# Kernel tuning notes

Measured on AMD Instinct MI355X. Metric: run time of the kernel, lower is better.

## Reference

```python
import jax, jax.numpy as jnp
from jax import lax
import numpy as np

# geomloss SamplesLoss(loss='sinkhorn', p=2, blur=0.01, scaling=0.7, debias=True),
# tensorized backend, single scale. Sinkhorn divergence with eps-scaling annealing.
P = 2
BLUR = 0.01
SCALING = 0.7
# geomloss estimates the diameter from the data at runtime; for jit-compatibility we
# use a fixed upper bound appropriate for N(0,1) data in D=64 (max pair dist ~ 18).
DIAMETER = 20.0


def eps_schedule():
    # geomloss epsilon_schedule(p, diameter, blur, scaling)
    eps_list = [DIAMETER ** P]
    eps_list += [float(np.exp(e)) for e in np.arange(P * np.log(DIAMETER), P * np.log(BLUR), P * np.log(SCALING))]
    eps_list += [BLUR ** P]
    return eps_list


def sq_cost(x, y):
    # C(x,y) = |x-y|^2 / 2  (geomloss cost for p=2)
    x2 = jnp.sum(x * x, axis=-1)
    y2 = jnp.sum(y * y, axis=-1)
    return 0.5 * (x2[:, None] + y2[None, :] - 2.0 * (x @ y.T))


def softmin(eps, C, h):
    # -eps * log sum_j exp(h_j - C_ij/eps), stable logsumexp over rows
    return -eps * jax.nn.logsumexp(h[None, :] - C / eps, axis=1)


def sinkhorn_divergence(x, y):
    N, M = x.shape[0], y.shape[0]
    dt = x.dtype
    a_log = jnp.full((N,), -np.log(N), dtype=dt)  # uniform weights, log
    b_log = jnp.full((M,), -np.log(M), dtype=dt)

    C_xy = sq_cost(x, y)
    C_yx = C_xy.T
    C_xx = sq_cost(x, x)
    C_yy = sq_cost(y, y)
    # geomloss runs the annealing loop without autograd; detach the costs.
    Dxy, Dyx = lax.stop_gradient(C_xy), lax.stop_gradient(C_yx)
    Dxx, Dyy = lax.stop_gradient(C_xx), lax.stop_gradient(C_yy)

    eps_list = eps_schedule()
    eps = eps_list[0]
    f_ba = softmin(eps, Dxy, b_log)  # potential on x-points wrt beta
    g_ab = softmin(eps, Dyx, a_log)  # potential on y-points wrt alpha
    f_aa = softmin(eps, Dxx, a_log)  # debias: self potentials
    g_bb = softmin(eps, Dyy, b_log)

    for eps in eps_list:  # symmetric Sinkhorn updates with averaging
        ft = softmin(eps, Dxy, b_log + g_ab / eps)
        gt = softmin(eps, Dyx, a_log + f_ba / eps)
        f_ba, g_ab = 0.5 * (f_ba + ft), 0.5 * (g_ab + gt)
        f_aa = 0.5 * (f_aa + softmin(eps, Dxx, a_log + f_aa / eps))
        g_bb = 0.5 * (g_bb + softmin(eps, Dyy, b_log + g_bb / eps))

    # final extrapolation at eps = blur^p with detached potentials (grads flow via C)
    eps = eps_list[-1]
    sg = lax.stop_gradient
    f_ba_n = softmin(eps, C_xy, sg(b_log + g_ab / eps))
    g_ab_n = softmin(eps, C_yx, sg(a_log + f_ba / eps))
    f_aa_n = softmin(eps, C_xx, sg(a_log + f_aa / eps))
    g_bb_n = softmin(eps, C_yy, sg(b_log + g_bb / eps))

    a = jnp.exp(a_log)
    b = jnp.exp(b_log)
    # debiased: <a, f_ab - f_aa> + <b, g_ba - g_bb>
    return jnp.sum(a * (f_ba_n - f_aa_n)) + jnp.sum(b * (g_ab_n - g_bb_n))


def setup_inputs() -> dict:
    key = jax.random.key(0)
    k1, k2 = jax.random.split(key)
    latentSource = jax.random.normal(k1, (4096, 64), dtype=jnp.float32)
    latentTarget = jax.random.normal(k2, (4096, 64), dtype=jnp.float32)
    return {"latentSource": latentSource, "latentTarget": latentTarget}


def reference(latentSource, latentTarget):
    return sinkhorn_divergence(latentSource, latentTarget)
```

## Files before the change

### kernel.cpp

```cpp
#include <hip/hip_runtime.h>
#include <hip/hip_bf16.h>
#include <math.h>

#define NPTS 4096
#define KD   64
#define BR   64
#define BC   128
#define NSPLIT 4
#define CT   (NPTS / (BC * NSPLIT))
#define NTHREADS 256
#define BLOG  (-8.317766166719343f)
#define BLOG2 (-12.0f)
#define LOG2E 1.4426950408889634f
#define LN2   0.6931471805599453f

typedef __bf16 bf16x8 __attribute__((ext_vector_type(8)));
typedef float  f32x4  __attribute__((ext_vector_type(4)));

__device__ __forceinline__ float ex2(float x) {
#if __has_builtin(__builtin_amdgcn_exp2f)
  return __builtin_amdgcn_exp2f(x);
#else
  return exp2f(x);
#endif
}
__device__ __forceinline__ float lg2(float x) {
#if __has_builtin(__builtin_amdgcn_logf)
  return __builtin_amdgcn_logf(x);
#else
  return log2f(x);
#endif
}

struct FusedArgs {
  const unsigned short* X[4];
  const unsigned short* Y[4];
  const float* csq[4];
  const float* pmr[4];
  const float* psr[4];
  const float* potr[4];
  float* potw[4];
  float* pm;
  float* ps;
  float ie2;
  float elp;
  float alpha, beta;
  int mode;
};

__device__ __forceinline__ void gll16(const void* g, void* l) {
  __builtin_amdgcn_global_load_lds(
      (const __attribute__((address_space(1))) void*)g,
      (__attribute__((address_space(3))) void*)l, 16, 0, 0);
}

__global__ __launch_bounds__(NTHREADS, 4)
void fused_softmin(FusedArgs A) {
  __shared__ __align__(16) __bf16 YT[2][BC * KD];
  __shared__ __align__(16) float QL[BC * CT];

  const int tid  = threadIdx.x;
  const int lane = tid & 63;
  const int wave = tid >> 6;
  const int ln16 = lane & 15;
  const int rg   = lane >> 4;
  const int ln7  = ln16 & 7;
  const int rowblk = blockIdx.x;
  const int split  = blockIdx.y;
  const int dir    = blockIdx.z;

  const __bf16* __restrict__ Xb = (const __bf16*)A.X[dir];
  const __bf16* __restrict__ Yb = (const __bf16*)A.Y[dir];
  const float ie2 = A.ie2;
  const int row0 = rowblk * BR;
  const int col0 = split * (CT * BC);

  const int srow = tid >> 3;
  const int sseg = tid & 7;

#pragma unroll
  for (int it = 0; it < 4; ++it) {
    int r = it * 32 + srow;
    gll16(Yb + (size_t)(col0 + r) * KD + ((sseg ^ (r & 7)) << 3),
          (__bf16*)YT[0] + it * 2048 + wave * 512);
  }

  bf16x8 af[2];
  {
    const __bf16* ap = Xb + (size_t)(row0 + wave * 16 + ln16) * KD + rg * 8;
#pragma unroll
    for (int ks = 0; ks < 2; ++ks) {
      union { uint4 u; bf16x8 v; } t;
      t.u = *(const uint4*)(ap + ks * 32);
      af[ks] = t.v;
    }
  }

  {
    const float* __restrict__ csq = A.csq[dir];
    if (A.mode == 0) {
#pragma unroll
      for (int i = 0; i < 4; ++i) {
        int c = col0 + tid + i * 256;
        QL[tid + i * 256] = BLOG2 - csq[c] * ie2;
      }
    } else {
      const float* __restrict__ pmr = A.pmr[dir];
      const float* __restrict__ psr = A.psr[dir];
      const float* __restrict__ potr = A.potr[dir];
      float* __restrict__ potw = A.potw[dir];
#pragma unroll
      for (int i = 0; i < 4; ++i) {
        int c = col0 + tid + i * 256;
        float m0 = pmr[0 * NPTS + c], m1 = pmr[1 * NPTS + c];
        float m2 = pmr[2 * NPTS + c], m3 = pmr[3 * NPTS + c];
        float s0 = psr[0 * NPTS + c], s1 = psr[1 * NPTS + c];
        float s2 = psr[2 * NPTS + c], s3 = psr[3 * NPTS + c];
        float m4 = fmaxf(fmaxf(m0, m1), fmaxf(m2, m3));
        float s4 = s0 * ex2(m0 - m4) + s1 * ex2(m1 - m4) +
                   s2 * ex2(m2 - m4) + s3 * ex2(m3 - m4);
        float lse2 = m4 + lg2(s4);
        float xsq = csq[c];
        float v = xsq - A.elp * lse2;
        float g = A.alpha * potr[c] + A.beta * v;
        if (rowblk == 0) potw[c] = g;
        QL[tid + i * 256] = BLOG2 + (g - xsq) * ie2;
      }
    }
  }

  float m[4], s[4];
#pragma unroll
  for (int r = 0; r < 4; ++r) { m[r] = -__builtin_inff(); s[r] = 0.f; }

  const __bf16* xbase_unused = nullptr; (void)xbase_unused;
  __syncthreads();

  for (int tile = 0; tile < CT; ++tile) {
    const int cb = tile & 1;

    if (tile < CT - 1) {
      const int nc0 = col0 + (tile + 1) * BC;
#pragma unroll
      for (int it = 0; it < 4; ++it) {
        int r = it * 32 + srow;
        gll16(Yb + (size_t)(nc0 + r) * KD + ((sseg ^ (r & 7)) << 3),
              (__bf16*)YT[cb ^ 1] + it * 2048 + wave * 512);
      }
    }

    float qv[8];
#pragma unroll
    for (int t = 0; t < 8; ++t) qv[t] = QL[tile * BC + t * 16 + ln16];

    f32x4 acc[8];
#pragma unroll
    for (int t = 0; t < 8; ++t)
#pragma unroll
      for (int i = 0; i < 4; ++i) acc[t][i] = 0.f;

    const __bf16* ybase = YT[cb] + ln16 * KD;
#pragma unroll
    for (int ks = 0; ks < 2; ++ks) {
      const int p = ((ks << 2) | rg) ^ ln7;
#pragma unroll
      for (int t = 0; t < 8; ++t) {
        union { uint4 u; bf16x8 v; } bb;
        bb.u = *(const uint4*)(ybase + t * 16 * KD + p * 8);
        acc[t] = __builtin_amdgcn_mfma_f32_16x16x32_bf16(af[ks], bb.v, acc[t], 0, 0, 0);
      }
    }

#pragma unroll
    for (int r = 0; r < 4; ++r) {
      float l[8];
#pragma unroll
      for (int t = 0; t < 8; ++t) l[t] = fmaf(acc[t][r], ie2, qv[t]);
      float tmax = -__builtin_inff();
#pragma unroll
      for (int t = 0; t < 8; ++t) tmax = fmaxf(tmax, l[t]);
      float mn = fmaxf(m[r], tmax);
      float sadd = 0.f;
#pragma unroll
      for (int t = 0; t < 8; ++t) sadd += ex2(l[t] - mn);
      s[r] = fmaf(s[r], ex2(m[r] - mn), sadd);
      m[r] = mn;
    }
    __syncthreads();
  }

#pragma unroll
  for (int r = 0; r < 4; ++r) {
#pragma unroll
    for (int d = 1; d < 16; d <<= 1) {
      float mo = __shfl_xor(m[r], d, 64);
      float so = __shfl_xor(s[r], d, 64);
      float mn = fmaxf(m[r], mo);
      s[r] = ex2(m[r] - mn) * s[r] + ex2(mo - mn) * so;
      m[r] = mn;
    }
  }
  if (ln16 == 0) {
#pragma unroll
    for (int r = 0; r < 4; ++r) {
      int row = row0 + wave * 16 + rg * 4 + r;
      size_t gi = (size_t)(dir * NSPLIT + split) * NPTS + row;
      A.pm[gi] = m[r];
      A.ps[gi] = s[r];
    }
  }
}

__global__ void prep(const float* __restrict__ x, const float* __restrict__ y,
                     float* xs, float* ys,
                     unsigned short* xb, unsigned short* yb) {
  int gid = blockIdx.x * blockDim.x + threadIdx.x;
  int isx = (gid < NPTS) ? 1 : 0;
  const float* p = isx ? x : y;
  int row = gid & (NPTS - 1);
  const float4* r4 = (const float4*)(p + (size_t)row * KD);
  unsigned short* ob = (isx ? xb : yb) + (size_t)row * KD;
  float s = 0.f;
#pragma unroll
  for (int i = 0; i < 16; ++i) {
    float4 v = r4[i];
    s += v.x * v.x + v.y * v.y + v.z * v.z + v.w * v.w;
    union { __bf16 h[4]; uint2 u; } t;
    t.h[0] = (__bf16)v.x; t.h[1] = (__bf16)v.y;
    t.h[2] = (__bf16)v.z; t.h[3] = (__bf16)v.w;
    *(uint2*)(ob + i * 4) = t.u;
  }
  (isx ? xs : ys)[row] = 0.5f * s;
}

__global__ void final_reduce(const float* __restrict__ pm,
                             const float* __restrict__ ps,
                             const float* __restrict__ xsx,
                             const float* __restrict__ xsy,
                             float elpF, float* out) {
  __shared__ float red[256];
  int t = threadIdx.x;
  float acc = 0.f;
  for (int r = t; r < NPTS; r += 256) {
#pragma unroll
    for (int d = 0; d < 4; ++d) {
      float m0 = pm[(size_t)(d * NSPLIT + 0) * NPTS + r];
      float m1 = pm[(size_t)(d * NSPLIT + 1) * NPTS + r];
      float m2 = pm[(size_t)(d * NSPLIT + 2) * NPTS + r];
      float m3 = pm[(size_t)(d * NSPLIT + 3) * NPTS + r];
      float s0 = ps[(size_t)(d * NSPLIT + 0) * NPTS + r];
      float s1 = ps[(size_t)(d * NSPLIT + 1) * NPTS + r];
      float s2 = ps[(size_t)(d * NSPLIT + 2) * NPTS + r];
      float s3 = ps[(size_t)(d * NSPLIT + 3) * NPTS + r];
      float m4 = fmaxf(fmaxf(m0, m1), fmaxf(m2, m3));
      float s4 = s0 * ex2(m0 - m4) + s1 * ex2(m1 - m4) +
                 s2 * ex2(m2 - m4) + s3 * ex2(m3 - m4);
      float lse2 = m4 + lg2(s4);
      float xsq = (d == 0 || d == 2) ? xsx[r] : xsy[r];
      float f = xsq - elpF * lse2;
      acc += (d < 2) ? f : -f;
    }
  }
  red[t] = acc;
  __syncthreads();
  for (int off = 128; off > 0; off >>= 1) {
    if (t < off) red[t] += red[t + off];
    __syncthreads();
  }
  if (t == 0) out[0] = red[0] * (1.0f / NPTS);
}

extern "C" void kernel_launch(void* const* d_in, const int* in_sizes, int n_in,
                              void* d_out, int out_size, void* d_ws, size_t ws_size,
                              hipStream_t stream) {
  const float* x = (const float*)d_in[0];
  const float* y = (const float*)d_in[1];
  float* out = (float*)d_out;
  float* w = (float*)d_ws;

  float* xs_x = w;
  float* xs_y = w + NPTS;
  float* pot0 = w + 2 * NPTS;
  float* pot1 = w + 6 * NPTS;
  float* pm0  = w + 10 * NPTS;
  float* ps0  = w + 26 * NPTS;
  float* pm1  = w + 42 * NPTS;
  float* ps1  = w + 58 * NPTS;
  unsigned short* xb = (unsigned short*)(w + 74 * NPTS);
  unsigned short* yb = (unsigned short*)(w + 106 * NPTS);
  float* pmb[2] = {pm0, pm1};
  float* psb[2] = {ps0, ps1};
  float* potb[2] = {pot0, pot1};

  double eps_list[32];
  int neps = 0;
  {
    double start = 2.0 * log(20.0);
    double stop  = 2.0 * log(0.01);
    double step  = 2.0 * log(0.7);
    eps_list[neps++] = 400.0;
    int cnt = (int)ceil((stop - start) / step);
    for (int i = 0; i < cnt && neps < 30; ++i) eps_list[neps++] = exp(start + (double)i * step);
    eps_list[neps++] = 1e-4;
  }

  const unsigned short* Xd[4] = {xb, yb, xb, yb};
  const unsigned short* Yd[4] = {yb, xb, xb, yb};
  const float* YSQd[4] = {xs_y, xs_x, xs_x, xs_y};
  const int qpair[4] = {1, 0, 2, 3};

  prep<<<dim3(32), dim3(256), 0, stream>>>(x, y, xs_x, xs_y, xb, yb);

  dim3 fgrid(NPTS / BR, NSPLIT, 4);

  double ecur[26];
  ecur[0] = eps_list[0];
  for (int k = 1; k <= 24; ++k) ecur[k] = eps_list[k - 1];
  ecur[25] = eps_list[neps - 1];

  for (int k = 0; k <= 25; ++k) {
    FusedArgs fa;
    for (int d = 0; d < 4; ++d) {
      fa.X[d] = Xd[d]; fa.Y[d] = Yd[d]; fa.csq[d] = YSQd[d];
      int p = qpair[d];
      fa.pmr[d]  = pmb[(k + 1) & 1] + (size_t)p * NSPLIT * NPTS;
      fa.psr[d]  = psb[(k + 1) & 1] + (size_t)p * NSPLIT * NPTS;
      fa.potr[d] = potb[(k + 1) & 1] + (size_t)p * NPTS;
      fa.potw[d] = potb[k & 1] + (size_t)p * NPTS;
    }
    fa.pm = pmb[k & 1];
    fa.ps = psb[k & 1];
    fa.ie2 = (float)(LOG2E / ecur[k]);
    fa.elp = (k == 0) ? 0.f : (float)(ecur[k - 1] * LN2);
    fa.alpha = (k <= 1) ? 0.f : 0.5f;
    fa.beta  = (k <= 1) ? 1.f : 0.5f;
    fa.mode  = (k == 0) ? 0 : 1;
    fused_softmin<<<fgrid, dim3(NTHREADS), 0, stream>>>(fa);
  }

  final_reduce<<<dim3(1), dim3(256), 0, stream>>>(
      pmb[25 & 1], psb[25 & 1], xs_x, xs_y,
      (float)(eps_list[neps - 1] * LN2), out);
}
```

Before: 636.8 us.

## Switch to 32x32x16 MFMA tiles and double row block per workgroup

The fused softmin kernel now uses 32x32x16 bf16 MFMA instructions instead of 16x16x32, and each wave covers 32 rows instead of 16, so the row block grows from 64 to 128. Each B fragment loaded from LDS now feeds more rows, which raises arithmetic intensity and halves the number of workgroups that reload the Y tiles. The online logsumexp state per lane grows to 16 rows and the cross-lane reduction widens to 32 lanes. This raises register pressure, so occupancy is lowered to 2 workgroups per CU, and the grid shrinks, which may underfill the GPU.

Result: slower. 750.4 us (+17.8%).

```diff
diff --git a/kernel.cpp b/kernel.cpp
--- a/kernel.cpp
+++ b/kernel.cpp
@@ -4,18 +4,17 @@
 
 #define NPTS 4096
 #define KD   64
-#define BR   64
+#define BR   128
 #define BC   128
 #define NSPLIT 4
 #define CT   (NPTS / (BC * NSPLIT))
 #define NTHREADS 256
-#define BLOG  (-8.317766166719343f)
 #define BLOG2 (-12.0f)
 #define LOG2E 1.4426950408889634f
 #define LN2   0.6931471805599453f
 
 typedef __bf16 bf16x8 __attribute__((ext_vector_type(8)));
-typedef float  f32x4  __attribute__((ext_vector_type(4)));
+typedef float  f32x16 __attribute__((ext_vector_type(16)));
 
 __device__ __forceinline__ float ex2(float x) {
 #if __has_builtin(__builtin_amdgcn_exp2f)
@@ -54,7 +53,7 @@
       (__attribute__((address_space(3))) void*)l, 16, 0, 0);
 }
 
-__global__ __launch_bounds__(NTHREADS, 4)
+__global__ __launch_bounds__(NTHREADS, 2)
 void fused_softmin(FusedArgs A) {
   __shared__ __align__(16) __bf16 YT[2][BC * KD];
   __shared__ __align__(16) float QL[BC * CT];
@@ -62,9 +61,9 @@
   const int tid  = threadIdx.x;
   const int lane = tid & 63;
   const int wave = tid >> 6;
-  const int ln16 = lane & 15;
-  const int rg   = lane >> 4;
-  const int ln7  = ln16 & 7;
+  const int ln   = lane & 31;
+  const int hh   = lane >> 5;
+  const int ln7  = ln & 7;
   const int rowblk = blockIdx.x;
   const int split  = blockIdx.y;
   const int dir    = blockIdx.z;
@@ -85,13 +84,13 @@
           (__bf16*)YT[0] + it * 2048 + wave * 512);
   }
 
-  bf16x8 af[2];
+  bf16x8 af[4];
   {
-    const __bf16* ap = Xb + (size_t)(row0 + wave * 16 + ln16) * KD + rg * 8;
-#pragma unroll
-    for (int ks = 0; ks < 2; ++ks) {
+    const __bf16* ap = Xb + (size_t)(row0 + wave * 32 + ln) * KD + hh * 8;
+#pragma unroll
+    for (int ks = 0; ks < 4; ++ks) {
       union { uint4 u; bf16x8 v; } t;
-      t.u = *(const uint4*)(ap + ks * 32);
+      t.u = *(const uint4*)(ap + ks * 16);
       af[ks] = t.v;
     }
   }
@@ -129,11 +128,10 @@
     }
   }
 
-  float m[4], s[4];
-#pragma unroll
-  for (int r = 0; r < 4; ++r) { m[r] = -__builtin_inff(); s[r] = 0.f; }
-
-  const __bf16* xbase_unused = nullptr; (void)xbase_unused;
+  float m[16], s[16];
+#pragma unroll
+  for (int r = 0; r < 16; ++r) { m[r] = -__builtin_inff(); s[r] = 0.f; }
+
   __syncthreads();
 
   for (int tile = 0; tile < CT; ++tile) {
@@ -149,40 +147,37 @@
       }
     }
 
-    float qv[8];
-#pragma unroll
-    for (int t = 0; t < 8; ++t) qv[t] = QL[tile * BC + t * 16 + ln16];
-
-    f32x4 acc[8];
-#pragma unroll
-    for (int t = 0; t < 8; ++t)
-#pragma unroll
-      for (int i = 0; i < 4; ++i) acc[t][i] = 0.f;
-
-    const __bf16* ybase = YT[cb] + ln16 * KD;
-#pragma unroll
-    for (int ks = 0; ks < 2; ++ks) {
-      const int p = ((ks << 2) | rg) ^ ln7;
-#pragma unroll
-      for (int t = 0; t < 8; ++t) {
+    float qv[4];
+#pragma unroll
+    for (int ct = 0; ct < 4; ++ct)
+      qv[ct] = QL[tile * BC + ct * 32 + ln];
+
+    f32x16 acc[4];
+#pragma unroll
+    for (int ct = 0; ct < 4; ++ct)
+#pragma unroll
+      for (int i = 0; i < 16; ++i) acc[ct][i] = 0.f;
+
+    const __bf16* ybase = YT[cb] + ln * KD;
+#pragma unroll
+    for (int ks = 0; ks < 4; ++ks) {
+      const int sg = ((ks << 1) | hh) ^ ln7;
+#pragma unroll
+      for (int ct = 0; ct < 4; ++ct) {
         union { uint4 u; bf16x8 v; } bb;
-        bb.u = *(const uint4*)(ybase + t * 16 * KD + p * 8);
-        acc[t] = __builtin_amdgcn_mfma_f32_16x16x32_bf16(af[ks], bb.v, acc[t], 0, 0, 0);
+        bb.u = *(const uint4*)(ybase + ct * 32 * KD + sg * 8);
+        acc[ct] = __builtin_amdgcn_mfma_f32_32x32x16_bf16(af[ks], bb.v, acc[ct], 0, 0, 0);
       }
     }
 
 #pragma unroll
-    for (int r = 0; r < 4; ++r) {
-      float l[8];
-#pragma unroll
-      for (int t = 0; t < 8; ++t) l[t] = fmaf(acc[t][r], ie2, qv[t]);
-      float tmax = -__builtin_inff();
-#pragma unroll
-      for (int t = 0; t < 8; ++t) tmax = fmaxf(tmax, l[t]);
-      float mn = fmaxf(m[r], tmax);
-      float sadd = 0.f;
-#pragma unroll
-      for (int t = 0; t < 8; ++t) sadd += ex2(l[t] - mn);
+    for (int r = 0; r < 16; ++r) {
+      float l0 = fmaf(acc[0][r], ie2, qv[0]);
+      float l1 = fmaf(acc[1][r], ie2, qv[1]);
+      float l2 = fmaf(acc[2][r], ie2, qv[2]);
+      float l3 = fmaf(acc[3][r], ie2, qv[3]);
+      float mn = fmaxf(m[r], fmaxf(fmaxf(l0, l1), fmaxf(l2, l3)));
+      float sadd = ex2(l0 - mn) + ex2(l1 - mn) + ex2(l2 - mn) + ex2(l3 - mn);
       s[r] = fmaf(s[r], ex2(m[r] - mn), sadd);
       m[r] = mn;
     }
@@ -190,9 +185,9 @@
   }
 
 #pragma unroll
-  for (int r = 0; r < 4; ++r) {
-#pragma unroll
-    for (int d = 1; d < 16; d <<= 1) {
+  for (int r = 0; r < 16; ++r) {
+#pragma unroll
+    for (int d = 1; d < 32; d <<= 1) {
       float mo = __shfl_xor(m[r], d, 64);
       float so = __shfl_xor(s[r], d, 64);
       float mn = fmaxf(m[r], mo);
@@ -200,10 +195,10 @@
       m[r] = mn;
     }
   }
-  if (ln16 == 0) {
-#pragma unroll
-    for (int r = 0; r < 4; ++r) {
-      int row = row0 + wave * 16 + rg * 4 + r;
+  if (ln == 0) {
+#pragma unroll
+    for (int r = 0; r < 16; ++r) {
+      int row = row0 + wave * 32 + (r & 3) + ((r >> 2) << 3) + (hh << 2);
       size_t gi = (size_t)(dir * NSPLIT + split) * NPTS + row;
       A.pm[gi] = m[r];
       A.ps[gi] = s[r];
```

## Reshape wave tiling to 32x64 per wave sharing B fragments across two row tiles

Applied to the files above, without the earlier changes.

Each wave now covers two 16-row tiles and half of the 128-column tile instead of one 16-row tile across all 128 columns. Each B fragment read from LDS feeds two MFMAs, which halves LDS reads per MFMA. Because the column halves are split across waves, the partial logsumexp count per row doubles from 4 to 8, so workspace, the merge step and the final reduce are widened to match. The launch bound is also switched to amdgpu_waves_per_eu(4,4). The cost is more per-lane register state and a larger partial merge.

Result: slower. 839.5 us (+31.8%).

```diff
diff --git a/kernel.cpp b/kernel.cpp
--- a/kernel.cpp
+++ b/kernel.cpp
@@ -7,9 +7,9 @@
 #define BR   64
 #define BC   128
 #define NSPLIT 4
+#define NPART  8
 #define CT   (NPTS / (BC * NSPLIT))
 #define NTHREADS 256
-#define BLOG  (-8.317766166719343f)
 #define BLOG2 (-12.0f)
 #define LOG2E 1.4426950408889634f
 #define LN2   0.6931471805599453f
@@ -54,7 +54,8 @@
       (__attribute__((address_space(3))) void*)l, 16, 0, 0);
 }
 
-__global__ __launch_bounds__(NTHREADS, 4)
+__global__ __launch_bounds__(NTHREADS)
+__attribute__((amdgpu_waves_per_eu(4, 4)))
 void fused_softmin(FusedArgs A) {
   __shared__ __align__(16) __bf16 YT[2][BC * KD];
   __shared__ __align__(16) float QL[BC * CT];
@@ -62,6 +63,8 @@
   const int tid  = threadIdx.x;
   const int lane = tid & 63;
   const int wave = tid >> 6;
+  const int rowgrp = wave >> 1;
+  const int half   = wave & 1;
   const int ln16 = lane & 15;
   const int rg   = lane >> 4;
   const int ln7  = ln16 & 7;
@@ -85,14 +88,15 @@
           (__bf16*)YT[0] + it * 2048 + wave * 512);
   }
 
-  bf16x8 af[2];
-  {
-    const __bf16* ap = Xb + (size_t)(row0 + wave * 16 + ln16) * KD + rg * 8;
+  bf16x8 af[2][2];
+#pragma unroll
+  for (int rt = 0; rt < 2; ++rt) {
+    const __bf16* ap = Xb + (size_t)(row0 + rowgrp * 32 + rt * 16 + ln16) * KD + rg * 8;
 #pragma unroll
     for (int ks = 0; ks < 2; ++ks) {
       union { uint4 u; bf16x8 v; } t;
       t.u = *(const uint4*)(ap + ks * 32);
-      af[ks] = t.v;
+      af[rt][ks] = t.v;
     }
   }
 
@@ -112,13 +116,17 @@
 #pragma unroll
       for (int i = 0; i < 4; ++i) {
         int c = col0 + tid + i * 256;
-        float m0 = pmr[0 * NPTS + c], m1 = pmr[1 * NPTS + c];
-        float m2 = pmr[2 * NPTS + c], m3 = pmr[3 * NPTS + c];
-        float s0 = psr[0 * NPTS + c], s1 = psr[1 * NPTS + c];
-        float s2 = psr[2 * NPTS + c], s3 = psr[3 * NPTS + c];
-        float m4 = fmaxf(fmaxf(m0, m1), fmaxf(m2, m3));
-        float s4 = s0 * ex2(m0 - m4) + s1 * ex2(m1 - m4) +
-                   s2 * ex2(m2 - m4) + s3 * ex2(m3 - m4);
+        float mv[NPART], sv[NPART];
+        float m4 = -__builtin_inff();
+#pragma unroll
+        for (int sp = 0; sp < NPART; ++sp) {
+          mv[sp] = pmr[sp * NPTS + c];
+          sv[sp] = psr[sp * NPTS + c];
+          m4 = fmaxf(m4, mv[sp]);
+        }
+        float s4 = 0.f;
+#pragma unroll
+        for (int sp = 0; sp < NPART; ++sp) s4 += sv[sp] * ex2(mv[sp] - m4);
         float lse2 = m4 + lg2(s4);
         float xsq = csq[c];
         float v = xsq - A.elp * lse2;
@@ -129,11 +137,12 @@
     }
   }
 
-  float m[4], s[4];
-#pragma unroll
-  for (int r = 0; r < 4; ++r) { m[r] = -__builtin_inff(); s[r] = 0.f; }
-
-  const __bf16* xbase_unused = nullptr; (void)xbase_unused;
+  float m[2][4], s[2][4];
+#pragma unroll
+  for (int rt = 0; rt < 2; ++rt)
+#pragma unroll
+    for (int r = 0; r < 4; ++r) { m[rt][r] = -__builtin_inff(); s[rt][r] = 0.f; }
+
   __syncthreads();
 
   for (int tile = 0; tile < CT; ++tile) {
@@ -149,65 +158,65 @@
       }
     }
 
-    float qv[8];
-#pragma unroll
-    for (int t = 0; t < 8; ++t) qv[t] = QL[tile * BC + t * 16 + ln16];
-
-    f32x4 acc[8];
-#pragma unroll
-    for (int t = 0; t < 8; ++t)
-#pragma unroll
-      for (int i = 0; i < 4; ++i) acc[t][i] = 0.f;
-
-    const __bf16* ybase = YT[cb] + ln16 * KD;
+    float qv[4];
+#pragma unroll
+    for (int ct = 0; ct < 4; ++ct)
+      qv[ct] = QL[tile * BC + half * 64 + ct * 16 + ln16];
+
+    f32x4 acc[2][4] = {};
+
+    const __bf16* yb0 = YT[cb] + (half * 64 + ln16) * KD;
 #pragma unroll
     for (int ks = 0; ks < 2; ++ks) {
       const int p = ((ks << 2) | rg) ^ ln7;
 #pragma unroll
-      for (int t = 0; t < 8; ++t) {
+      for (int ct = 0; ct < 4; ++ct) {
         union { uint4 u; bf16x8 v; } bb;
-        bb.u = *(const uint4*)(ybase + t * 16 * KD + p * 8);
-        acc[t] = __builtin_amdgcn_mfma_f32_16x16x32_bf16(af[ks], bb.v, acc[t], 0, 0, 0);
-      }
-    }
-
+        bb.u = *(const uint4*)(yb0 + ct * 16 * KD + p * 8);
+        acc[0][ct] = __builtin_amdgcn_mfma_f32_16x16x32_bf16(af[0][ks], bb.v, acc[0][ct], 0, 0, 0);
+        acc[1][ct] = __builtin_amdgcn_mfma_f32_16x16x32_bf16(af[1][ks], bb.v, acc[1][ct], 0, 0, 0);
+      }
+    }
+
+#pragma unroll
+    for (int rt = 0; rt < 2; ++rt)
+#pragma unroll
+      for (int r = 0; r < 4; ++r) {
+        float l0 = fmaf(acc[rt][0][r], ie2, qv[0]);
+        float l1 = fmaf(acc[rt][1][r], ie2, qv[1]);
+        float l2 = fmaf(acc[rt][2][r], ie2, qv[2]);
+        float l3 = fmaf(acc[rt][3][r], ie2, qv[3]);
+        float mn = fmaxf(m[rt][r], fmaxf(fmaxf(l0, l1), fmaxf(l2, l3)));
+        float sadd = ex2(l0 - mn) + ex2(l1 - mn) + ex2(l2 - mn) + ex2(l3 - mn);
+        s[rt][r] = fmaf(s[rt][r], ex2(m[rt][r] - mn), sadd);
+        m[rt][r] = mn;
+      }
+    __syncthreads();
+  }
+
+#pragma unroll
+  for (int rt = 0; rt < 2; ++rt)
 #pragma unroll
     for (int r = 0; r < 4; ++r) {
-      float l[8];
-#pragma unroll
-      for (int t = 0; t < 8; ++t) l[t] = fmaf(acc[t][r], ie2, qv[t]);
-      float tmax = -__builtin_inff();
-#pragma unroll
-      for (int t = 0; t < 8; ++t) tmax = fmaxf(tmax, l[t]);
-      float mn = fmaxf(m[r], tmax);
-      float sadd = 0.f;
-#pragma unroll
-      for (int t = 0; t < 8; ++t) sadd += ex2(l[t] - mn);
-      s[r] = fmaf(s[r], ex2(m[r] - mn), sadd);
-      m[r] = mn;
-    }
-    __syncthreads();
-  }
-
-#pragma unroll
-  for (int r = 0; r < 4; ++r) {
-#pragma unroll
-    for (int d = 1; d < 16; d <<= 1) {
-      float mo = __shfl_xor(m[r], d, 64);
-      float so = __shfl_xor(s[r], d, 64);
-      float mn = fmaxf(m[r], mo);
-      s[r] = ex2(m[r] - mn) * s[r] + ex2(mo - mn) * so;
-      m[r] = mn;
-    }
-  }
+#pragma unroll
+      for (int d = 1; d < 16; d <<= 1) {
+        float mo = __shfl_xor(m[rt][r], d, 64);
+        float so = __shfl_xor(s[rt][r], d, 64);
+        float mn = fmaxf(m[rt][r], mo);
+        s[rt][r] = ex2(m[rt][r] - mn) * s[rt][r] + ex2(mo - mn) * so;
+        m[rt][r] = mn;
+      }
+    }
   if (ln16 == 0) {
 #pragma unroll
-    for (int r = 0; r < 4; ++r) {
-      int row = row0 + wave * 16 + rg * 4 + r;
-      size_t gi = (size_t)(dir * NSPLIT + split) * NPTS + row;
-      A.pm[gi] = m[r];
-      A.ps[gi] = s[r];
-    }
+    for (int rt = 0; rt < 2; ++rt)
+#pragma unroll
+      for (int r = 0; r < 4; ++r) {
+        int row = row0 + rowgrp * 32 + rt * 16 + rg * 4 + r;
+        size_t gi = (size_t)(dir * NPART + split * 2 + half) * NPTS + row;
+        A.pm[gi] = m[rt][r];
+        A.ps[gi] = s[rt][r];
+      }
   }
 }
 
@@ -244,17 +253,17 @@
   for (int r = t; r < NPTS; r += 256) {
 #pragma unroll
     for (int d = 0; d < 4; ++d) {
-      float m0 = pm[(size_t)(d * NSPLIT + 0) * NPTS + r];
-      float m1 = pm[(size_t)(d * NSPLIT + 1) * NPTS + r];
-      float m2 = pm[(size_t)(d * NSPLIT + 2) * NPTS + r];
-      float m3 = pm[(size_t)(d * NSPLIT + 3) * NPTS + r];
-      float s0 = ps[(size_t)(d * NSPLIT + 0) * NPTS + r];
-      float s1 = ps[(size_t)(d * NSPLIT + 1) * NPTS + r];
-      float s2 = ps[(size_t)(d * NSPLIT + 2) * NPTS + r];
-      float s3 = ps[(size_t)(d * NSPLIT + 3) * NPTS + r];
-      float m4 = fmaxf(fmaxf(m0, m1), fmaxf(m2, m3));
-      float s4 = s0 * ex2(m0 - m4) + s1 * ex2(m1 - m4) +
-                 s2 * ex2(m2 - m4) + s3 * ex2(m3 - m4);
+      float mv[NPART], sv[NPART];
+      float m4 = -__builtin_inff();
+#pragma unroll
+      for (int sp = 0; sp < NPART; ++sp) {
+        mv[sp] = pm[(size_t)(d * NPART + sp) * NPTS + r];
+        sv[sp] = ps[(size_t)(d * NPART + sp) * NPTS + r];
+        m4 = fmaxf(m4, mv[sp]);
+      }
+      float s4 = 0.f;
+#pragma unroll
+      for (int sp = 0; sp < NPART; ++sp) s4 += sv[sp] * ex2(mv[sp] - m4);
       float lse2 = m4 + lg2(s4);
       float xsq = (d == 0 || d == 2) ? xsx[r] : xsy[r];
       float f = xsq - elpF * lse2;
@@ -283,11 +292,11 @@
   float* pot0 = w + 2 * NPTS;
   float* pot1 = w + 6 * NPTS;
   float* pm0  = w + 10 * NPTS;
-  float* ps0  = w + 26 * NPTS;
-  float* pm1  = w + 42 * NPTS;
-  float* ps1  = w + 58 * NPTS;
-  unsigned short* xb = (unsigned short*)(w + 74 * NPTS);
-  unsigned short* yb = (unsigned short*)(w + 106 * NPTS);
+  float* ps0  = w + 42 * NPTS;
+  float* pm1  = w + 74 * NPTS;
+  float* ps1  = w + 106 * NPTS;
+  unsigned short* xb = (unsigned short*)(w + 138 * NPTS);
+  unsigned short* yb = (unsigned short*)(w + 170 * NPTS);
   float* pmb[2] = {pm0, pm1};
   float* psb[2] = {ps0, ps1};
   float* potb[2] = {pot0, pot1};
@@ -323,8 +332,8 @@
     for (int d = 0; d < 4; ++d) {
       fa.X[d] = Xd[d]; fa.Y[d] = Yd[d]; fa.csq[d] = YSQd[d];
       int p = qpair[d];
-      fa.pmr[d]  = pmb[(k + 1) & 1] + (size_t)p * NSPLIT * NPTS;
-      fa.psr[d]  = psb[(k + 1) & 1] + (size_t)p * NSPLIT * NPTS;
+      fa.pmr[d]  = pmb[(k + 1) & 1] + (size_t)p * NPART * NPTS;
+      fa.psr[d]  = psb[(k + 1) & 1] + (size_t)p * NPART * NPTS;
       fa.potr[d] = potb[(k + 1) & 1] + (size_t)p * NPTS;
       fa.potw[d] = potb[k & 1] + (size_t)p * NPTS;
     }
```
